# Optimization experiments

Hardware: AMD Instinct MI355X
Metric: run time of the kernel (lower is better)

## Reference

```python
import jax, jax.numpy as jnp
import numpy as np

N = 100000
E = 1000000
C = 64      # hidden_channels
H = 4       # heads
O = C // H  # out channels per head
NEG_SLOPE = 0.2


def setup_inputs() -> dict:
    key = jax.random.key(0)
    ks = jax.random.split(key, 14)
    x = jax.random.normal(ks[0], (N, C), dtype=jnp.float32)
    edge_index = jax.random.randint(ks[1], (2, E), 0, N, dtype=jnp.int64)
    s = 1.0 / np.sqrt(C)
    params = {}
    for l in range(3):
        params[f"Wl{l+1}"] = jax.random.normal(ks[2 + 4 * l], (C, H * O), dtype=jnp.float32) * s
        params[f"Wr{l+1}"] = jax.random.normal(ks[3 + 4 * l], (C, H * O), dtype=jnp.float32) * s
        params[f"a{l+1}"] = jax.random.normal(ks[4 + 4 * l], (H, O), dtype=jnp.float32) * s
        params[f"b{l+1}"] = jnp.zeros((H * O,), dtype=jnp.float32)
    return {"x": x, "edge_index": edge_index, **params}


def _gatv2_layer(x, src, dst, Wl, Wr, a, b):
    # x: [N, C]; src/dst: [E]
    xl = (x @ Wl).reshape(N, H, O)  # source-side transform
    xr = (x @ Wr).reshape(N, H, O)  # target-side transform
    s = jax.nn.leaky_relu(xl[src] + xr[dst], NEG_SLOPE)     # [E, H, O]
    e = jnp.einsum("eho,ho->eh", s, a)                       # [E, H] logits
    # segment softmax over incoming edges of each target node
    m = jax.ops.segment_max(e, dst, num_segments=N)          # [N, H]
    ex = jnp.exp(e - m[dst])
    denom = jax.ops.segment_sum(ex, dst, num_segments=N)     # [N, H]
    alpha = ex / (denom[dst] + 1e-16)                        # [E, H]
    out = jax.ops.segment_sum(xl[src] * alpha[:, :, None], dst, num_segments=N)
    return out.reshape(N, H * O) + b


def reference(x, edge_index, Wl1, Wr1, a1, b1, Wl2, Wr2, a2, b2, Wl3, Wr3, a3, b3):
    src, dst = edge_index[0], edge_index[1]
    h = jax.nn.relu(_gatv2_layer(x, src, dst, Wl1, Wr1, a1, b1))
    h = jax.nn.relu(_gatv2_layer(h, src, dst, Wl2, Wr2, a2, b2))
    h = _gatv2_layer(h, src, dst, Wl3, Wr3, a3, b3)
    return h
```

## Files before the change

kernel.cpp:

```cpp
#include <hip/hip_runtime.h>
#include <math.h>

#define SLOPE 0.2f
#define LOG2E 1.4426950408889634f

#define DPP_ADD(x, ctrl) \
    ((x) + __int_as_float(__builtin_amdgcn_update_dpp( \
        0, __float_as_int(x), (ctrl), 0xF, 0xF, true)))


#define NPB 256
#define EPB 8192
#define MAXBK 2048

__global__ __launch_bounds__(256) void kH1(const int* __restrict__ ei,
                                           int* __restrict__ hist,
                                           int E, int nbk, int nblkE) {
    __shared__ int h[MAXBK];
    int t = threadIdx.x, b = blockIdx.x;
    for (int i = t; i < nbk; i += 256) h[i] = 0;
    __syncthreads();
    int e0 = b * EPB, e1 = min(e0 + EPB, E);
    for (int e = e0 + t; e < e1; e += 256)
        atomicAdd(&h[ei[E + e] >> 8], 1);
    __syncthreads();
    for (int i = t; i < nbk; i += 256)
        hist[i * nblkE + b] = h[i];
}

__global__ __launch_bounds__(256) void kH2(const int* __restrict__ ei,
                                           const int* __restrict__ hs,
                                           int* __restrict__ pairs,
                                           int E, int nbk, int nblkE) {
    __shared__ int soff[MAXBK];
    int t = threadIdx.x, b = blockIdx.x;
    for (int i = t; i < nbk; i += 256) soff[i] = hs[i * nblkE + b];
    __syncthreads();
    int e0 = b * EPB, e1 = min(e0 + EPB, E);
    for (int e = e0 + t; e < e1; e += 256) {
        int s = ei[e], d = ei[E + e];
        int slot = atomicAdd(&soff[d >> 8], 1);
        pairs[slot] = (s << 8) | (d & (NPB - 1));
    }
}

__global__ __launch_bounds__(256) void kB3(const int* __restrict__ hs,
                                           const int* __restrict__ pairs,
                                           int* __restrict__ btot,
                                           int E, int nbk, int nblkE) {
    __shared__ int sdeg[NPB];
    __shared__ int red[256];
    int t = threadIdx.x, b = blockIdx.x;
    sdeg[t] = 0;
    __syncthreads();
    int s0 = hs[b * nblkE];
    int s1 = (b + 1 < nbk) ? hs[(b + 1) * nblkE] : E;
    for (int i = s0 + t; i < s1; i += 256)
        atomicAdd(&sdeg[pairs[i] & (NPB - 1)], 1);
    __syncthreads();
    red[t] = (sdeg[t] + 3) & ~3;
    __syncthreads();
    for (int off = 128; off; off >>= 1) {
        if (t < off) red[t] += red[t + off];
        __syncthreads();
    }
    if (t == 0) btot[b] = red[0];
}

__global__ __launch_bounds__(256) void kscanB(const int* __restrict__ btot,
                                              int* __restrict__ bbase, int nbk) {
    __shared__ int sd[256];
    __shared__ int carry;
    int t = threadIdx.x;
    if (t == 0) carry = 0;
    __syncthreads();
    for (int base = 0; base < nbk; base += 256) {
        int v = (base + t < nbk) ? btot[base + t] : 0;
        sd[t] = v;
        __syncthreads();
        for (int off = 1; off < 256; off <<= 1) {
            int x = (t >= off) ? sd[t - off] : 0;
            __syncthreads();
            sd[t] += x;
            __syncthreads();
        }
        if (base + t < nbk) bbase[base + t] = sd[t] - v + carry;
        __syncthreads();
        if (t == 255) carry += sd[255];
        __syncthreads();
    }
}

__global__ __launch_bounds__(256) void kB4(const int* __restrict__ hs,
                                           const int* __restrict__ pairs,
                                           const int* __restrict__ bbase,
                                           int* __restrict__ rp,
                                           int* __restrict__ deg,
                                           int* __restrict__ col,
                                           int E, int nbk, int nblkE, int n) {
    __shared__ int sdeg[NPB];
    __shared__ int spfx[NPB];
    int t = threadIdx.x, b = blockIdx.x;
    sdeg[t] = 0;
    __syncthreads();
    int s0 = hs[b * nblkE];
    int s1 = (b + 1 < nbk) ? hs[(b + 1) * nblkE] : E;
    for (int i = s0 + t; i < s1; i += 256)
        atomicAdd(&sdeg[pairs[i] & (NPB - 1)], 1);
    __syncthreads();
    int cnt = sdeg[t];
    int pv = (cnt + 3) & ~3;
    spfx[t] = pv;
    __syncthreads();
    for (int off = 1; off < 256; off <<= 1) {
        int x = (t >= off) ? spfx[t - off] : 0;
        __syncthreads();
        spfx[t] += x;
        __syncthreads();
    }
    int rpt = bbase[b] + spfx[t] - pv;
    int node = b * NPB + t;
    if (node < n) { rp[node] = rpt; deg[node] = cnt; }
    __syncthreads();
    sdeg[t] = rpt;
    __syncthreads();
    for (int i = s0 + t; i < s1; i += 256) {
        int p = pairs[i];
        int slot = atomicAdd(&sdeg[p & (NPB - 1)], 1);
        col[slot] = p & ~(NPB - 1);
    }
}


__global__ __launch_bounds__(256) void k_scan1(const int* __restrict__ deg,
                                               int* __restrict__ rp,
                                               int* __restrict__ blk, int n) {
    __shared__ int sd[256];
    int t = threadIdx.x;
    int base = blockIdx.x * 1024 + t * 4;
    int v0 = 0, v1 = 0, v2 = 0, v3 = 0;
    if (base + 0 < n) v0 = deg[base + 0];
    if (base + 1 < n) v1 = deg[base + 1];
    if (base + 2 < n) v2 = deg[base + 2];
    if (base + 3 < n) v3 = deg[base + 3];
    int s = v0 + v1 + v2 + v3;
    sd[t] = s;
    __syncthreads();
    for (int off = 1; off < 256; off <<= 1) {
        int x = (t >= off) ? sd[t - off] : 0;
        __syncthreads();
        sd[t] += x;
        __syncthreads();
    }
    int ex = sd[t] - s;
    if (t == 255) blk[blockIdx.x] = sd[255];
    if (base + 0 < n) rp[base + 0] = ex; ex += v0;
    if (base + 1 < n) rp[base + 1] = ex; ex += v1;
    if (base + 2 < n) rp[base + 2] = ex; ex += v2;
    if (base + 3 < n) rp[base + 3] = ex;
}

__global__ __launch_bounds__(256) void k_scan2(int* __restrict__ blk, int nblk) {
    __shared__ int sd[256];
    int t = threadIdx.x;
    int v = (t < nblk) ? blk[t] : 0;
    sd[t] = v;
    __syncthreads();
    for (int off = 1; off < 256; off <<= 1) {
        int x = (t >= off) ? sd[t - off] : 0;
        __syncthreads();
        sd[t] += x;
        __syncthreads();
    }
    if (t < nblk) blk[t] = sd[t] - v;
}

__global__ __launch_bounds__(256) void k_scan3(int* __restrict__ rp,
                                               const int* __restrict__ blk,
                                               int n) {
    int t = threadIdx.x;
    int base = blockIdx.x * 1024 + t * 4;
    int off = blk[blockIdx.x];
    #pragma unroll
    for (int i = 0; i < 4; i++) {
        int idx = base + i;
        if (idx < n) rp[idx] += off;
    }
}


__global__ __launch_bounds__(256) void k_gemm(const float* __restrict__ in,
                                              const float* __restrict__ Wl,
                                              const float* __restrict__ Wr,
                                              float* __restrict__ xl,
                                              float* __restrict__ xr, int n) {
    __shared__ float4 sW[64 * 32];
    __shared__ float  sx[64 * 68];

    int t = threadIdx.x;
    int base = blockIdx.x * 64;

    float4 xs[4];
    int xrow[4], xkq[4];
    #pragma unroll
    for (int s = 0; s < 4; s++) {
        int i = t + 256 * s;
        int row = i >> 4, kq = i & 15;
        int g = base + row;
        if (g > n - 1) g = n - 1;
        xs[s] = *(const float4*)(in + (size_t)g * 64 + kq * 4);
        xrow[s] = row; xkq[s] = kq;
    }
    for (int i = t; i < 2048; i += 256) {
        int k = i >> 5, jg = i & 31;
        const float* src = (jg < 16) ? (Wl + k * 64 + jg * 4)
                                     : (Wr + k * 64 + (jg - 16) * 4);
        sW[i] = *(const float4*)src;
    }
    #pragma unroll
    for (int s = 0; s < 4; s++)
        *(float4*)(sx + xrow[s] * 68 + xkq[s] * 4) = xs[s];
    __syncthreads();

    int rt = t & 15;
    int ct = t >> 4;
    const float* sxp = sx + rt * 68;

    float4 acc[4][2];
    #pragma unroll
    for (int r = 0; r < 4; r++)
        #pragma unroll
        for (int j = 0; j < 2; j++) acc[r][j] = make_float4(0.f, 0.f, 0.f, 0.f);

    #pragma unroll 1
    for (int k0 = 0; k0 < 64; k0 += 4) {
        float4 xv[4];
        #pragma unroll
        for (int r = 0; r < 4; r++)
            xv[r] = *(const float4*)(sxp + r * (16 * 68) + k0);
        #pragma unroll
        for (int kk = 0; kk < 4; kk++) {
            float4 w0 = sW[(k0 + kk) * 32 + ct * 2 + 0];
            float4 w1 = sW[(k0 + kk) * 32 + ct * 2 + 1];
            #pragma unroll
            for (int r = 0; r < 4; r++) {
                float xk = (kk == 0) ? xv[r].x : (kk == 1) ? xv[r].y
                         : (kk == 2) ? xv[r].z : xv[r].w;
                acc[r][0].x += xk * w0.x;
                acc[r][0].y += xk * w0.y;
                acc[r][0].z += xk * w0.z;
                acc[r][0].w += xk * w0.w;
                acc[r][1].x += xk * w1.x;
                acc[r][1].y += xk * w1.y;
                acc[r][1].z += xk * w1.z;
                acc[r][1].w += xk * w1.w;
            }
        }
    }

    float* outh = (ct < 8) ? xl : xr;
    int cq = (ct & 7) * 8;
    #pragma unroll
    for (int r = 0; r < 4; r++) {
        int g = base + rt + 16 * r;
        if (g < n) {
            float* dst = outh + (size_t)g * 64 + cq;
            *(float4*)(dst + 0) = acc[r][0];
            *(float4*)(dst + 4) = acc[r][1];
        }
    }
}


__global__ __launch_bounds__(256) void k_node(const float* __restrict__ xl,
                                              const float* __restrict__ xr,
                                              const int* __restrict__ rp,
                                              const int* __restrict__ deg,
                                              const int* __restrict__ col,
                                              const float* __restrict__ A,
                                              const float* __restrict__ Bv,
                                              float* __restrict__ outp,
                                              int n, int relu) {
    int lane = threadIdx.x & 63;
    int node = __builtin_amdgcn_readfirstlane(blockIdx.x * 4 + (threadIdx.x >> 6));
    if (node >= n) return;
    unsigned lane4 = (unsigned)lane * 4u;

    float xr_d = xr[(size_t)node * 64 + lane];
    float a_l = A[lane] * LOG2E;
    float b_l = Bv[lane];

    int start = rp[node];
    int d = deg[node];
    int nb = (d + 7) >> 3;
    const int* cp = col + start;
    const char* xlb = (const char*)xl;

    float den = 0.f, acc = 0.f;

    auto batch = [&](const float (&v)[8], int valid) {
        float p[8];
        #pragma unroll
        for (int j = 0; j < 8; j++) {
            float s = v[j] + xr_d;
            s = fmaxf(s, SLOPE * s);
            float q = s * a_l;
            q = DPP_ADD(q, 0xB1);
            q = DPP_ADD(q, 0x4E);
            q = DPP_ADD(q, 0x141);
            q = DPP_ADD(q, 0x140);
            p[j] = q;
        }
        if (valid < 8) {
            #pragma unroll
            for (int j = 0; j < 8; j++)
                if (j >= valid) p[j] = -INFINITY;
        }
        #pragma unroll
        for (int j = 0; j < 8; j++) {
            float w = __builtin_amdgcn_exp2f(p[j]);
            den += w;
            acc += w * v[j];
        }
    };

    float v[8];
    if (nb > 0) {
        int c[8];
        *(int4*)(c + 0) = *(const int4*)(cp + 0);
        *(int4*)(c + 4) = *(const int4*)(cp + 4);
        #pragma unroll
        for (int j = 0; j < 8; j++)
            v[j] = *(const float*)(xlb + ((unsigned)c[j] + lane4));
    }

    #pragma unroll 1
    for (int b = 0; b < nb - 1; b++) {
        int cN[8];
        float vN[8];
        const int* q = cp + (b + 1) * 8;
        *(int4*)(cN + 0) = *(const int4*)(q + 0);
        *(int4*)(cN + 4) = *(const int4*)(q + 4);
        #pragma unroll
        for (int j = 0; j < 8; j++)
            vN[j] = *(const float*)(xlb + ((unsigned)cN[j] + lane4));

        batch(v, 8);

        #pragma unroll
        for (int j = 0; j < 8; j++) v[j] = vN[j];
    }

    if (nb > 0) {
        batch(v, d - (nb - 1) * 8);
    }

    float o = acc / (den + 1e-16f) + b_l;
    if (relu) o = fmaxf(o, 0.f);
    outp[(size_t)node * 64 + lane] = o;
}


extern "C" void kernel_launch(void* const* d_in, const int* in_sizes, int n_in,
                              void* d_out, int out_size, void* d_ws, size_t ws_size,
                              hipStream_t stream) {
    const float* x = (const float*)d_in[0];
    const int* ei = (const int*)d_in[1];
    int N = in_sizes[0] / 64;
    int E = in_sizes[1] / 2;

    const float* Wl[3] = {(const float*)d_in[2], (const float*)d_in[6], (const float*)d_in[10]};
    const float* Wr[3] = {(const float*)d_in[3], (const float*)d_in[7], (const float*)d_in[11]};
    const float* Av[3] = {(const float*)d_in[4], (const float*)d_in[8], (const float*)d_in[12]};
    const float* Bv[3] = {(const float*)d_in[5], (const float*)d_in[9], (const float*)d_in[13]};

    char* w = (char*)d_ws;
    auto carve = [&](size_t bytes) {
        void* p = (void*)w;
        w += (bytes + 255) & ~(size_t)255;
        return p;
    };
    int NBK    = (N + NPB - 1) / NPB;
    int NBLK_E = (E + EPB - 1) / EPB;
    size_t histN = (size_t)NBK * NBLK_E;
    size_t colN = (size_t)E + 3 * (size_t)N + 64;
    float* xl    = (float*)carve((size_t)N * 64 * 4);
    float* xr    = (float*)carve((size_t)N * 64 * 4);
    float* h     = (float*)carve((size_t)N * 64 * 4);
    int*   rp    = (int*)carve((size_t)N * 4);
    int*   deg   = (int*)carve((size_t)N * 4);
    int*   col   = (int*)carve(colN * 4);
    int*   pairs = (int*)carve((size_t)E * 4);
    int*   hist  = (int*)carve(histN * 4);
    int*   hs    = (int*)carve(histN * 4);
    int*   btot  = (int*)carve((size_t)NBK * 4);
    int*   bbase = (int*)carve((size_t)NBK * 4);
    int*   blkB  = (int*)carve(256 * 4);

    int nblkH1024 = (int)((histN + 1023) / 1024);
    int gemm_grid = (N + 63) / 64;
    int node_grid = (N + 3) / 4;

    hipMemsetAsync(col, 0, colN * 4, stream);

    kH1<<<NBLK_E, 256, 0, stream>>>(ei, hist, E, NBK, NBLK_E);
    k_scan1<<<nblkH1024, 256, 0, stream>>>(hist, hs, blkB, (int)histN);
    k_scan2<<<1, 256, 0, stream>>>(blkB, nblkH1024);
    k_scan3<<<nblkH1024, 256, 0, stream>>>(hs, blkB, (int)histN);
    kH2<<<NBLK_E, 256, 0, stream>>>(ei, hs, pairs, E, NBK, NBLK_E);

    kB3<<<NBK, 256, 0, stream>>>(hs, pairs, btot, E, NBK, NBLK_E);
    kscanB<<<1, 256, 0, stream>>>(btot, bbase, NBK);
    kB4<<<NBK, 256, 0, stream>>>(hs, pairs, bbase, rp, deg, col, E, NBK, NBLK_E, N);

    const float* in_l = x;
    for (int l = 0; l < 3; l++) {
        float* out_l = (l == 2) ? (float*)d_out : h;
        int relu = (l < 2) ? 1 : 0;
        k_gemm<<<gemm_grid, 256, 0, stream>>>(in_l, Wl[l], Wr[l], xl, xr, N);
        k_node<<<node_grid, 256, 0, stream>>>(xl, xr, rp, deg, col, Av[l], Bv[l],
                                              out_l, N, relu);
        in_l = h;
    }
}
```

Measured before the change: 379.5 us.

## Split wavefront into two half-waves each gathering float2 per lane for alternate edges

The per-node aggregation kernel now has each 32-lane half of the wavefront process alternating edges, with each lane loading two channels as a float2 instead of one float. The per-head dot-product reduction uses one fewer DPP step, and the two halves' softmax partials are combined with a cross-half shuffle at the end. This halves the number of gather instructions and exp evaluations per edge and doubles the load width. In exchange it adds a channel remapping, tail masking per half, and a final shuffle; the online softmax still skips max subtraction as before.

After: 359.6 us. 5.2% less time.

```diff
diff --git a/kernel.cpp b/kernel.cpp
--- a/kernel.cpp
+++ b/kernel.cpp
@@ -284,11 +284,15 @@
     int lane = threadIdx.x & 63;
     int node = __builtin_amdgcn_readfirstlane(blockIdx.x * 4 + (threadIdx.x >> 6));
     if (node >= n) return;
-    unsigned lane4 = (unsigned)lane * 4u;
-
-    float xr_d = xr[(size_t)node * 64 + lane];
-    float a_l = A[lane] * LOG2E;
-    float b_l = Bv[lane];
+    int grp = lane >> 5;
+    int s   = lane & 31;
+    int chn = ((s >> 3) << 4) + ((s & 7) << 1);
+    unsigned cofs = (unsigned)chn * 4u;
+
+    float2 xr2 = *(const float2*)(xr + (size_t)node * 64 + chn);
+    float2 a2  = *(const float2*)(A + chn);
+    a2.x *= LOG2E; a2.y *= LOG2E;
+    float2 b2  = *(const float2*)(Bv + chn);
 
     int start = rp[node];
     int d = deg[node];
@@ -296,68 +300,65 @@
     const int* cp = col + start;
     const char* xlb = (const char*)xl;
 
-    float den = 0.f, acc = 0.f;
-
-    auto batch = [&](const float (&v)[8], int valid) {
-        float p[8];
-        #pragma unroll
-        for (int j = 0; j < 8; j++) {
-            float s = v[j] + xr_d;
-            s = fmaxf(s, SLOPE * s);
-            float q = s * a_l;
+    float den = 0.f;
+    float ax = 0.f, ay = 0.f;
+
+    auto batch = [&](const float2 (&v)[4], int ebase, bool full) {
+        #pragma unroll
+        for (int j = 0; j < 4; j++) {
+            float sx_ = v[j].x + xr2.x;
+            float sy_ = v[j].y + xr2.y;
+            sx_ = fmaxf(sx_, SLOPE * sx_);
+            sy_ = fmaxf(sy_, SLOPE * sy_);
+            float q = sx_ * a2.x + sy_ * a2.y;
             q = DPP_ADD(q, 0xB1);
             q = DPP_ADD(q, 0x4E);
             q = DPP_ADD(q, 0x141);
-            q = DPP_ADD(q, 0x140);
-            p[j] = q;
-        }
-        if (valid < 8) {
-            #pragma unroll
-            for (int j = 0; j < 8; j++)
-                if (j >= valid) p[j] = -INFINITY;
-        }
-        #pragma unroll
-        for (int j = 0; j < 8; j++) {
-            float w = __builtin_amdgcn_exp2f(p[j]);
+            if (!full) {
+                int eidx = ebase + 2 * j + grp;
+                if (eidx >= d) q = -INFINITY;
+            }
+            float w = __builtin_amdgcn_exp2f(q);
             den += w;
-            acc += w * v[j];
+            ax += w * v[j].x;
+            ay += w * v[j].y;
         }
     };
 
-    float v[8];
-    if (nb > 0) {
+    auto gather = [&](float2 (&v)[4], const int* q) {
         int c[8];
-        *(int4*)(c + 0) = *(const int4*)(cp + 0);
-        *(int4*)(c + 4) = *(const int4*)(cp + 4);
-        #pragma unroll
-        for (int j = 0; j < 8; j++)
-            v[j] = *(const float*)(xlb + ((unsigned)c[j] + lane4));
-    }
+        *(int4*)(c + 0) = *(const int4*)(q + 0);
+        *(int4*)(c + 4) = *(const int4*)(q + 4);
+        #pragma unroll
+        for (int j = 0; j < 4; j++) {
+            unsigned cc = (unsigned)(grp ? c[2 * j + 1] : c[2 * j]);
+            v[j] = *(const float2*)(xlb + (cc + cofs));
+        }
+    };
+
+    float2 v[4];
+    if (nb > 0) gather(v, cp);
 
     #pragma unroll 1
     for (int b = 0; b < nb - 1; b++) {
-        int cN[8];
-        float vN[8];
-        const int* q = cp + (b + 1) * 8;
-        *(int4*)(cN + 0) = *(const int4*)(q + 0);
-        *(int4*)(cN + 4) = *(const int4*)(q + 4);
-        #pragma unroll
-        for (int j = 0; j < 8; j++)
-            vN[j] = *(const float*)(xlb + ((unsigned)cN[j] + lane4));
-
-        batch(v, 8);
-
-        #pragma unroll
-        for (int j = 0; j < 8; j++) v[j] = vN[j];
-    }
-
-    if (nb > 0) {
-        batch(v, d - (nb - 1) * 8);
-    }
-
-    float o = acc / (den + 1e-16f) + b_l;
-    if (relu) o = fmaxf(o, 0.f);
-    outp[(size_t)node * 64 + lane] = o;
+        float2 vN[4];
+        gather(vN, cp + (b + 1) * 8);
+        batch(v, b * 8, true);
+        #pragma unroll
+        for (int j = 0; j < 4; j++) v[j] = vN[j];
+    }
+    if (nb > 0) batch(v, (nb - 1) * 8, false);
+
+    den += __shfl_xor(den, 32, 64);
+    ax  += __shfl_xor(ax, 32, 64);
+    ay  += __shfl_xor(ay, 32, 64);
+
+    float inv = 1.f / (den + 1e-16f);
+    float ox = ax * inv + b2.x;
+    float oy = ay * inv + b2.y;
+    if (relu) { ox = fmaxf(ox, 0.f); oy = fmaxf(oy, 0.f); }
+    if (grp == 0)
+        *(float2*)(outp + (size_t)node * 64 + chn) = make_float2(ox, oy);
 }
 
 
```
